# Performance work log

Measured on AMD Instinct MI355X. Metric: run time of the kernel, lower is better.

Reference implementation:

```python
import jax, jax.numpy as jnp
import numpy as np

B, N, F_IN = 8, 4096, 128
H0, H1, OUT = 64, 32, 32
DENSITY = 0.004  # avg degree ~16


def setup_inputs() -> dict:
    key = jax.random.key(0)
    ks = jax.random.split(key, 8)
    x = jax.random.normal(ks[0], (B, N, F_IN), dtype=jnp.float32)
    # sparse binary adjacency (graph structure), stored dense as the module does
    adj = (jax.random.uniform(ks[1], (B, N, N)) < DENSITY).astype(jnp.float32)
    def w(k, i, o):
        return jax.random.normal(k, (i, o), dtype=jnp.float32) * (1.0 / np.sqrt(i))
    return {
        "x": x, "adj": adj,
        "Ws0": w(ks[2], F_IN, H0), "Wn0": w(ks[3], F_IN, H0), "b0": jnp.zeros((H0,), jnp.float32),
        "Ws1": w(ks[4], H0, H1),   "Wn1": w(ks[5], H0, H1),   "b1": jnp.zeros((H1,), jnp.float32),
        "Ws2": w(ks[6], H1, OUT),  "Wn2": w(ks[7], H1, OUT),  "b2": jnp.zeros((OUT,), jnp.float32),
    }


def _sage_layer(h, adj, deg_inv, Ws, Wn, b):
    # mean over incoming neighbors: row j of adj selects messages into node j
    neigh = jnp.einsum('bij,bjd->bid', adj, h) * deg_inv  # [B,N,d_in]
    return jax.nn.relu(h @ Ws + neigh @ Wn + b)


def reference(x, adj, Ws0, Wn0, b0, Ws1, Wn1, b1, Ws2, Wn2, b2):
    deg = jnp.sum(adj, axis=-1, keepdims=True)  # [B,N,1] in-degree
    deg_inv = 1.0 / jnp.maximum(deg, 1.0)
    h = _sage_layer(x, adj, deg_inv, Ws0, Wn0, b0)
    h = _sage_layer(h, adj, deg_inv, Ws1, Wn1, b1)
    h = _sage_layer(h, adj, deg_inv, Ws2, Wn2, b2)
    # original flattens to [B*N, out_dim] embeddings
    return h.reshape(B * N, -1)
```

## Files before the change

### kernel.cpp

```cpp
#include <hip/hip_runtime.h>
#include <hip/hip_bf16.h>

#define BN      32768
#define NCOL    4096
#define MAX_NBR 64

#define WS_NBR 0
#define WS_DEG (4*1024*1024)
#define WS_H0  (WS_DEG + 131072)
#define WS_H1  (WS_H0 + 8*1024*1024)

__global__ __launch_bounds__(256) void build_csr_kernel(
    const float* __restrict__ adj,
    unsigned short* __restrict__ nbr,
    int* __restrict__ deg)
{
    const int wave = threadIdx.x >> 6, lane = threadIdx.x & 63;
    const int row  = (blockIdx.x << 2) + wave;
    const float4* arow = reinterpret_cast<const float4*>(adj + (size_t)row * NCOL);
    unsigned short* outrow = nbr + (size_t)row * MAX_NBR;
    const unsigned long long below = (1ull << lane) - 1ull;

    int cnt = 0;
    #pragma unroll 4
    for (int t = 0; t < 16; ++t) {
        const int c = t * 64 + lane;
        const float4 q = arow[c];
        const float v[4] = { q.x, q.y, q.z, q.w };
        #pragma unroll
        for (int e = 0; e < 4; ++e) {
            const bool nz = (v[e] != 0.0f);
            const unsigned long long m = __ballot(nz);
            if (nz) {
                const int pos = cnt + (int)__popcll(m & below);
                if (pos < MAX_NBR) outrow[pos] = (unsigned short)(c * 4 + e);
            }
            cnt += (int)__popcll(m);
        }
    }
    if (lane == 0) deg[row] = cnt;
}

template<int D_IN, int D_OUT>
__global__ __launch_bounds__(256) void gather_layer_kernel(
    const float* __restrict__ hin,
    const unsigned short* __restrict__ nbr,
    const int* __restrict__ deg,
    const float* __restrict__ Ws, const float* __restrict__ Wn,
    const float* __restrict__ bias,
    float* __restrict__ hout)
{
    constexpr int SUB = (D_IN >= 64) ? 1 : (64 / D_IN);
    constexpr int KPL = (D_IN + 63) / 64;
    constexpr int NW  = 4 * SUB;
    __shared__ float s_self[D_IN];
    __shared__ float s_part[NW][D_IN];
    __shared__ float s_neigh[D_IN];

    const int tid  = threadIdx.x;
    const int wave = tid >> 6, lane = tid & 63;
    const int sub  = (D_IN < 64) ? (lane / D_IN) : 0;
    const int sl   = (D_IN < 64) ? (lane % D_IN) : lane;
    const int strm = wave * SUB + sub;
    const int row  = blockIdx.x;
    const int jbase = row & ~(NCOL - 1);

    const int d   = deg[row];
    const int cnt = d < MAX_NBR ? d : MAX_NBR;
    const float dinv = 1.0f / (float)(d > 1 ? d : 1);

    int mycol = 0;
    if (lane < cnt) mycol = nbr[(size_t)row * MAX_NBR + lane];

    if (wave == 0) {
        if constexpr (KPL == 2) {
            const float2 f = *(const float2*)(hin + (size_t)row * D_IN + 2 * lane);
            s_self[2 * lane] = f.x; s_self[2 * lane + 1] = f.y;
        } else {
            if (lane < D_IN) s_self[lane] = hin[(size_t)row * D_IN + lane];
        }
    }

    float nv[KPL];
    #pragma unroll
    for (int i = 0; i < KPL; ++i) nv[i] = 0.f;
    for (int t = strm; t < cnt; t += NW) {
        const int j = jbase + __shfl(mycol, t, 64);
        if constexpr (KPL == 2) {
            const float2 f = *(const float2*)(hin + (size_t)j * D_IN + 2 * lane);
            nv[0] += f.x; nv[1] += f.y;
        } else {
            nv[0] += hin[(size_t)j * D_IN + sl];
        }
    }
    if constexpr (KPL == 2) {
        s_part[strm][2 * lane]     = nv[0];
        s_part[strm][2 * lane + 1] = nv[1];
    } else {
        s_part[strm][sl] = nv[0];
    }
    __syncthreads();

    if (tid < D_IN) {
        float s = 0.f;
        #pragma unroll
        for (int p = 0; p < NW; ++p) s += s_part[p][tid];
        s_neigh[tid] = s * dinv;
    }
    __syncthreads();

    if (wave == 0) {
        constexpr int SEG  = 64 / D_OUT;
        constexpr int KSEG = D_IN / SEG;
        const int o = lane % D_OUT, seg = lane / D_OUT;
        float acc = 0.f;
        #pragma unroll 8
        for (int kk = 0; kk < KSEG; ++kk) {
            const int k = seg * KSEG + kk;
            acc = fmaf(s_self[k],  Ws[k * D_OUT + o], acc);
            acc = fmaf(s_neigh[k], Wn[k * D_OUT + o], acc);
        }
        if constexpr (SEG == 2) acc += __shfl_xor(acc, 32, 64);
        if (seg == 0)
            hout[(size_t)row * D_OUT + o] = fmaxf(acc + bias[o], 0.f);
    }
}

extern "C" void kernel_launch(void* const* d_in, const int* in_sizes, int n_in,
                              void* d_out, int out_size, void* d_ws, size_t ws_size,
                              hipStream_t stream) {
    const float* x   = (const float*)d_in[0];
    const float* adj = (const float*)d_in[1];
    const float* Ws0 = (const float*)d_in[2]; const float* Wn0 = (const float*)d_in[3];
    const float* b0  = (const float*)d_in[4];
    const float* Ws1 = (const float*)d_in[5]; const float* Wn1 = (const float*)d_in[6];
    const float* b1  = (const float*)d_in[7];
    const float* Ws2 = (const float*)d_in[8]; const float* Wn2 = (const float*)d_in[9];
    const float* b2  = (const float*)d_in[10];

    char* ws = (char*)d_ws;
    unsigned short* nbr = (unsigned short*)(ws + WS_NBR);
    int*   deg = (int*)(ws + WS_DEG);
    float* h0  = (float*)(ws + WS_H0);
    float* h1  = (float*)(ws + WS_H1);

    build_csr_kernel<<<BN / 4, 256, 0, stream>>>(adj, nbr, deg);
    gather_layer_kernel<128, 64><<<BN, 256, 0, stream>>>(
        x,  nbr, deg, Ws0, Wn0, b0, h0);
    gather_layer_kernel<64, 32><<<BN, 256, 0, stream>>>(
        h0, nbr, deg, Ws1, Wn1, b1, h1);
    gather_layer_kernel<32, 32><<<BN, 256, 0, stream>>>(
        h1, nbr, deg, Ws2, Wn2, b2, (float*)d_out);
}
```

Before: 908.4 us.

## Build CSR via LDS atomics and interleave gather rows across batches

The CSR build replaces the per-element ballot/popcount compaction with integer nonzero tests and LDS atomic appends, then writes the list out coalesced. Neighbor order within a row becomes nondeterministic, which reorders the float summation. The gather kernels also remap blockIdx so consecutive blocks cover different batches, spreading concurrent blocks across the eight batches' feature rows. The main cost targeted is ALU and ballot work in the bandwidth-bound scan of the 512MB adjacency.

```diff
diff --git a/kernel.cpp b/kernel.cpp
--- a/kernel.cpp
+++ b/kernel.cpp
@@ -15,29 +15,33 @@
     unsigned short* __restrict__ nbr,
     int* __restrict__ deg)
 {
+    __shared__ int s_cnt[4];
+    __shared__ unsigned short s_list[4][MAX_NBR];
     const int wave = threadIdx.x >> 6, lane = threadIdx.x & 63;
     const int row  = (blockIdx.x << 2) + wave;
-    const float4* arow = reinterpret_cast<const float4*>(adj + (size_t)row * NCOL);
-    unsigned short* outrow = nbr + (size_t)row * MAX_NBR;
-    const unsigned long long below = (1ull << lane) - 1ull;
+    if (lane == 0) s_cnt[wave] = 0;
+    __syncthreads();
 
-    int cnt = 0;
-    #pragma unroll 4
+    const uint4* arow = reinterpret_cast<const uint4*>(adj + (size_t)row * NCOL);
+    #pragma unroll
     for (int t = 0; t < 16; ++t) {
-        const int c = t * 64 + lane;
-        const float4 q = arow[c];
-        const float v[4] = { q.x, q.y, q.z, q.w };
-        #pragma unroll
-        for (int e = 0; e < 4; ++e) {
-            const bool nz = (v[e] != 0.0f);
-            const unsigned long long m = __ballot(nz);
-            if (nz) {
-                const int pos = cnt + (int)__popcll(m & below);
-                if (pos < MAX_NBR) outrow[pos] = (unsigned short)(c * 4 + e);
-            }
-            cnt += (int)__popcll(m);
+        const uint4 q = arow[t * 64 + lane];
+        if (q.x | q.y | q.z | q.w) {
+            const int c4 = (t * 64 + lane) * 4;
+            if (q.x) { int p = atomicAdd(&s_cnt[wave], 1);
+                       if (p < MAX_NBR) s_list[wave][p] = (unsigned short)(c4    ); }
+            if (q.y) { int p = atomicAdd(&s_cnt[wave], 1);
+                       if (p < MAX_NBR) s_list[wave][p] = (unsigned short)(c4 + 1); }
+            if (q.z) { int p = atomicAdd(&s_cnt[wave], 1);
+                       if (p < MAX_NBR) s_list[wave][p] = (unsigned short)(c4 + 2); }
+            if (q.w) { int p = atomicAdd(&s_cnt[wave], 1);
+                       if (p < MAX_NBR) s_list[wave][p] = (unsigned short)(c4 + 3); }
         }
     }
+    __syncthreads();
+    const int cnt = s_cnt[wave];
+    const int cl  = cnt < MAX_NBR ? cnt : MAX_NBR;
+    if (lane < cl) nbr[(size_t)row * MAX_NBR + lane] = s_list[wave][lane];
     if (lane == 0) deg[row] = cnt;
 }
 
@@ -62,7 +66,7 @@
     const int sub  = (D_IN < 64) ? (lane / D_IN) : 0;
     const int sl   = (D_IN < 64) ? (lane % D_IN) : lane;
     const int strm = wave * SUB + sub;
-    const int row  = blockIdx.x;
+    const int row  = ((blockIdx.x & 7) << 12) | (blockIdx.x >> 3);
     const int jbase = row & ~(NCOL - 1);
 
     const int d   = deg[row];
```

Measured after the change: 863.6 us. 1.05x faster.
